# Optimization experiments

Hardware: AMD Instinct MI355X
Metric: run time of the kernel (lower is better)

## Reference

```python
import jax, jax.numpy as jnp
import numpy as np

TEMPERATURE = 0.07
THRESHOLD = 0.7
NUM = 21          # config['data_loader']['args']['class_num']
EPS = 1e-12       # F.normalize eps
NEG_BIG = 1e30


def _nearest_down(x, H, W):
    # torch F.interpolate(mode='nearest'): in_idx = floor(out_idx * in/out)
    Hin, Win = x.shape[-2], x.shape[-1]
    ih = (jnp.arange(H) * Hin) // H
    iw = (jnp.arange(W) * Win) // W
    return x[..., ih[:, None], iw[None, :]]


def _l2n(x):
    return x / jnp.maximum(jnp.linalg.norm(x, axis=1, keepdims=True), EPS)


def setup_inputs() -> dict:
    key = jax.random.key(0)
    ks = jax.random.split(key, 6)
    B, C, H, W = 8, 256, 128, 128
    return {
        "labels": jax.random.randint(ks[0], (B, 512, 512), 0, NUM, dtype=jnp.int64)
        if jax.config.jax_enable_x64 else jax.random.randint(ks[0], (B, 512, 512), 0, NUM, dtype=jnp.int32),
        "features_old": jax.random.normal(ks[1], (B, C, H, W), dtype=jnp.float32),
        "features": jax.random.normal(ks[2], (B, C, H, W), dtype=jnp.float32),
        "outputs_old": jax.random.normal(ks[3], (B, 16, 512, 512), dtype=jnp.float32),
        "outputs": jax.random.normal(ks[4], (B, NUM, 512, 512), dtype=jnp.float32),
        "prototypes": jax.random.normal(ks[5], (NUM, C), dtype=jnp.float32),
        "num_class": 21,
        "num_old_class": 16,
        "num_new_class": 5,
        "epoch": 1,
        "train_step": 1,
        "len_epoch": 100,
    }


def reference(labels, features_old, features, outputs_old, outputs, prototypes,
              num_class, num_old_class, num_new_class, epoch, train_step, len_epoch):
    B, C, H, W = features.shape
    f32 = features.dtype

    # pseudo-label construction
    labels_down = _nearest_down(labels, H, W)                      # [B,H,W] int
    bgr_mask = (labels_down == 0).astype(labels_down.dtype)
    oo = jnp.where(outputs_old < THRESHOLD, 0.0, outputs_old)
    old_pred = jnp.argmax(oo, axis=1)                              # [B,512,512]
    old_down = _nearest_down(old_pred, H, W).astype(labels_down.dtype)
    pseudo = old_down * bgr_mask + labels_down                     # [B,H,W]
    lab = pseudo.reshape(-1)                                       # [N]
    mask = (lab >= 0) & (lab < NUM)

    # [N, C] normalized pixel features
    fa = _l2n(features.transpose(0, 2, 3, 1).reshape(-1, C))
    fo = _l2n(features_old.transpose(0, 2, 3, 1).reshape(-1, C))

    # per-class mean (segment reduce) replacing the python loop over unique labels
    seg = jnp.where(mask, lab, NUM)
    w = mask.astype(f32)
    counts = jax.ops.segment_sum(w, seg, num_segments=NUM + 1)[:NUM]          # [K]
    sum_a = jax.ops.segment_sum(fa * w[:, None], seg, num_segments=NUM + 1)[:NUM]
    sum_o = jax.ops.segment_sum(fo * w[:, None], seg, num_segments=NUM + 1)[:NUM]
    present = counts > 0
    denom = jnp.where(present, counts, 1.0)[:, None]
    anc = jnp.where(present[:, None], sum_a / denom, 0.0)          # [K,C] anchor prototypes
    con_prev = jnp.where(present[:, None], sum_o / denom, 0.0)     # [K,C] old prototypes
    contrast = jax.lax.stop_gradient(jnp.concatenate([anc, con_prev], axis=0))  # [2K,C]

    K = NUM
    eye = jnp.eye(K, dtype=f32)
    rowp = present.astype(f32)                                     # [K]
    colp = jnp.concatenate([rowp, rowp])                           # [2K]
    # labels are unique per row, so R = [I | I]; pos = [0 | I]; neg = 1 - R
    pos_mask = jnp.concatenate([jnp.zeros((K, K), f32), eye], axis=1) * rowp[:, None] * colp[None, :]
    neg_mask = (1.0 - jnp.concatenate([eye, eye], axis=1)) * rowp[:, None] * colp[None, :]

    adc = (anc @ contrast.T) / TEMPERATURE                         # [K,2K]
    # NOTE: faithful to source, negatives use UNshifted logits
    neg = jnp.sum(jnp.exp(adc) * neg_mask, axis=1, keepdims=True)  # [K,1]
    logits_max = jnp.max(jnp.where(colp[None, :] > 0, adc, -NEG_BIG), axis=1, keepdims=True)
    shifted = adc - jax.lax.stop_gradient(logits_max)
    pos_contrast = shifted * pos_mask - jnp.log(jnp.exp(shifted) + neg) * pos_mask

    num = pos_mask.sum(axis=1)
    valid = num > 0
    row_loss = -pos_contrast.sum(axis=1) / jnp.where(valid, num, 1.0)
    loss = jnp.sum(jnp.where(valid, row_loss, 0.0)) / jnp.maximum(jnp.sum(valid.astype(f32)), 1.0)
    return loss
```

## Files before the change

### kernel.cpp

```cpp
#include <hip/hip_runtime.h>
#include <math.h>

#define NPIX   131072
#define CCH    256
#define HW     16384
#define BSTR   4194304
#define NUMC   21
#define KC     5376
#define NREP   16

typedef __attribute__((ext_vector_type(8))) short bf16x8;
typedef __attribute__((ext_vector_type(4))) float f32x4;

static __device__ __forceinline__ uint f2bf(float x) {
    uint u = __builtin_bit_cast(uint, x);
    return (u + 0x7FFFu + ((u >> 16) & 1u)) >> 16;
}
static __device__ __forceinline__ uint oh(int lbl, int cls) {
    return (lbl == cls) ? 0x3F80u : 0u;
}

__global__ __launch_bounds__(256) void k_labels(const int* __restrict__ labels,
                                                const float* __restrict__ outputs_old,
                                                int* __restrict__ lab,
                                                float* __restrict__ gcnt)
{
    __shared__ float cnt[NUMC];
    if (threadIdx.x < NUMC) cnt[threadIdx.x] = 0.f;
    __syncthreads();

    int p = blockIdx.x * 256 + threadIdx.x;
    int b = p >> 14;
    int rem = p & 16383;
    int h = rem >> 7;
    int w = rem & 127;
    int ld = labels[b * 262144 + (h * 4) * 512 + (w * 4)];
    int out = ld;
    if (ld == 0) {
        const float* oo = outputs_old + (size_t)b * BSTR + (size_t)(h * 4) * 512 + (w * 4);
        float v0 = oo[0];
        float best = (v0 < 0.7f) ? 0.0f : v0;
        int bi = 0;
        #pragma unroll
        for (int c = 1; c < 16; ++c) {
            float v = oo[(size_t)c * 262144];
            v = (v < 0.7f) ? 0.0f : v;
            if (v > best) { best = v; bi = c; }
        }
        out = bi;
    }
    lab[p] = out;
    unsafeAtomicAdd(&cnt[out], 1.0f);
    __syncthreads();
    if (threadIdx.x < NUMC) unsafeAtomicAdd(&gcnt[threadIdx.x], cnt[threadIdx.x]);
}

__global__ __launch_bounds__(256, 4) void k_msum(const float* __restrict__ fa,
                                                 const float* __restrict__ fo,
                                                 const int* __restrict__ lab,
                                                 float* __restrict__ partA,
                                                 float* __restrict__ partO)
{
    __shared__ ushort tile[32 * 256];
    __shared__ float4 ssqP4[32];
    __shared__ int    labS[256];

    const int t = threadIdx.x;
    const int w = t >> 6, l = t & 63;
    const int isO = blockIdx.x & 1;
    const float* __restrict__ src = isO ? fo : fa;
    float* part = isO ? partO : partA;

    const int pbase = (blockIdx.x >> 1) * 256;
    const int img   = pbase >> 14;
    const int hw0   = pbase & 16383;
    const float* g  = src + (size_t)img * BSTR + hw0;

    labS[t] = lab[pbase + t];

    const int chb = w * 8 + (l >> 3);
    const int pq  = l & 7;

    f32x4 acc[2][4];
    #pragma unroll
    for (int m = 0; m < 2; ++m)
        #pragma unroll
        for (int n = 0; n < 4; ++n)
            acc[m][n] = (f32x4){0.f, 0.f, 0.f, 0.f};

    float4 v[8];
    #pragma unroll
    for (int i = 0; i < 8; ++i)
        v[i] = *(const float4*)(g + (size_t)(chb + 32 * i) * HW + pq * 4);

    for (int ph = 0; ph < 8; ++ph) {
        float4 s = {0.f, 0.f, 0.f, 0.f};
        #pragma unroll
        for (int i = 0; i < 8; ++i) {
            s.x += v[i].x * v[i].x;  s.y += v[i].y * v[i].y;
            s.z += v[i].z * v[i].z;  s.w += v[i].w * v[i].w;
        }
        #pragma unroll
        for (int off = 8; off < 64; off <<= 1) {
            s.x += __shfl_xor(s.x, off, 64);
            s.y += __shfl_xor(s.y, off, 64);
            s.z += __shfl_xor(s.z, off, 64);
            s.w += __shfl_xor(s.w, off, 64);
        }
        if (l < 8) ssqP4[w * 8 + l] = make_float4(s.x, s.y, s.z, s.w);
        __syncthreads();
        float4 q0 = ssqP4[pq],      q1 = ssqP4[8 + pq];
        float4 q2 = ssqP4[16 + pq], q3 = ssqP4[24 + pq];
        float4 inv;
        inv.x = 1.0f / fmaxf(sqrtf(q0.x + q1.x + q2.x + q3.x), 1e-12f);
        inv.y = 1.0f / fmaxf(sqrtf(q0.y + q1.y + q2.y + q3.y), 1e-12f);
        inv.z = 1.0f / fmaxf(sqrtf(q0.z + q1.z + q2.z + q3.z), 1e-12f);
        inv.w = 1.0f / fmaxf(sqrtf(q0.w + q1.w + q2.w + q3.w), 1e-12f);

        #pragma unroll
        for (int i = 0; i < 8; ++i) {
            uint lo = f2bf(v[i].x * inv.x) | (f2bf(v[i].y * inv.y) << 16);
            uint hi = f2bf(v[i].z * inv.z) | (f2bf(v[i].w * inv.w) << 16);
            int ch = chb + 32 * i;
            *(uint2*)&tile[(((pq >> 1) * 256 + ch) << 3) + ((pq & 1) << 2)] =
                make_uint2(lo, hi);
        }
        if (ph < 7) {
            #pragma unroll
            for (int i = 0; i < 8; ++i)
                v[i] = *(const float4*)(g + (size_t)(chb + 32 * i) * HW + (ph + 1) * 32 + pq * 4);
        }
        __syncthreads();

        const int base = ph * 32 + ((l >> 4) << 3);
        int4 la = *(const int4*)&labS[base];
        int4 lb = *(const int4*)&labS[base + 4];
        const int cls0 = l & 15, cls1 = 16 + (l & 15);
        uint4 u0, u1;
        u0.x = oh(la.x, cls0) | (oh(la.y, cls0) << 16);
        u0.y = oh(la.z, cls0) | (oh(la.w, cls0) << 16);
        u0.z = oh(lb.x, cls0) | (oh(lb.y, cls0) << 16);
        u0.w = oh(lb.z, cls0) | (oh(lb.w, cls0) << 16);
        u1.x = oh(la.x, cls1) | (oh(la.y, cls1) << 16);
        u1.y = oh(la.z, cls1) | (oh(la.w, cls1) << 16);
        u1.z = oh(lb.x, cls1) | (oh(lb.y, cls1) << 16);
        u1.w = oh(lb.z, cls1) | (oh(lb.w, cls1) << 16);
        bf16x8 A0 = __builtin_bit_cast(bf16x8, u0);
        bf16x8 A1 = __builtin_bit_cast(bf16x8, u1);

        #pragma unroll
        for (int n = 0; n < 4; ++n) {
            const int ct = w * 4 + n;
            const bf16x8 B = *(const bf16x8*)&tile[((l >> 4) * 256 + ct * 16 + (l & 15)) << 3];
            acc[0][n] = __builtin_amdgcn_mfma_f32_16x16x32_bf16(A0, B, acc[0][n], 0, 0, 0);
            acc[1][n] = __builtin_amdgcn_mfma_f32_16x16x32_bf16(A1, B, acc[1][n], 0, 0, 0);
        }
    }

    const int rep = (blockIdx.x >> 1) & (NREP - 1);
    #pragma unroll
    for (int m = 0; m < 2; ++m)
        #pragma unroll
        for (int n = 0; n < 4; ++n) {
            const int col = (w * 4 + n) * 16 + (l & 15);
            #pragma unroll
            for (int r = 0; r < 4; ++r) {
                const int row = m * 16 + (l >> 4) * 4 + r;
                if (row < NUMC)
                    unsafeAtomicAdd(&part[rep * KC + row * 256 + col], acc[m][n][r]);
            }
        }
}

__global__ __launch_bounds__(256) void k_final(const float* __restrict__ partA,
                                               const float* __restrict__ partO,
                                               const float* __restrict__ gcnt,
                                               float* __restrict__ out)
{
    __shared__ float anc[NUMC * 260];
    __shared__ float con[NUMC * 260];
    __shared__ float adc[NUMC * 44];
    __shared__ float cntS[NUMC];
    __shared__ float rowloss[NUMC];
    __shared__ float rowvalid[NUMC];

    if (threadIdx.x < NUMC) cntS[threadIdx.x] = gcnt[threadIdx.x];
    __syncthreads();
    for (int i = threadIdx.x; i < KC; i += 256) {
        float sA = 0.f, sO = 0.f;
        #pragma unroll
        for (int r = 0; r < NREP; ++r) { sA += partA[r * KC + i]; sO += partO[r * KC + i]; }
        int k = i >> 8, c = i & 255;
        float cn = cntS[k];
        bool pr = cn > 0.f;
        float d = pr ? cn : 1.f;
        anc[k * 260 + c] = pr ? sA / d : 0.f;
        con[k * 260 + c] = pr ? sO / d : 0.f;
    }
    __syncthreads();
    for (int pair = threadIdx.x; pair < NUMC * 2 * NUMC; pair += 256) {
        int k = pair / (2 * NUMC);
        int j = pair % (2 * NUMC);
        const float* ar = anc + k * 260;
        const float* br = (j < NUMC) ? (anc + j * 260) : (con + (j - NUMC) * 260);
        float s = 0.f;
        for (int c = 0; c < CCH; c += 4) {
            float4 a4 = *(const float4*)(ar + c);
            float4 b4 = *(const float4*)(br + c);
            s += a4.x * b4.x + a4.y * b4.y + a4.z * b4.z + a4.w * b4.w;
        }
        adc[k * 44 + j] = s / 0.07f;
    }
    __syncthreads();
    if (threadIdx.x < NUMC) {
        int k = threadIdx.x;
        bool pr = cntS[k] > 0.f;
        float neg = 0.f;
        float mx = -1e30f;
        for (int j = 0; j < 2 * NUMC; ++j) {
            int cj = (j < NUMC) ? j : (j - NUMC);
            bool cp = cntS[cj] > 0.f;
            float v = adc[k * 44 + j];
            if (cp) {
                if (v > mx) mx = v;
                if (j != k && j != NUMC + k) neg += expf(v);
            }
        }
        float sh = adc[k * 44 + NUMC + k] - mx;
        float rl = -(sh - logf(expf(sh) + neg));
        rowloss[k] = pr ? rl : 0.f;
        rowvalid[k] = pr ? 1.f : 0.f;
    }
    __syncthreads();
    if (threadIdx.x == 0) {
        float s = 0.f, v = 0.f;
        for (int kk = 0; kk < NUMC; ++kk) { s += rowloss[kk]; v += rowvalid[kk]; }
        out[0] = s / fmaxf(v, 1.f);
    }
}

extern "C" void kernel_launch(void* const* d_in, const int* in_sizes, int n_in,
                              void* d_out, int out_size, void* d_ws, size_t ws_size,
                              hipStream_t stream) {
    const int*   labels      = (const int*)  d_in[0];
    const float* feats_old   = (const float*)d_in[1];
    const float* feats       = (const float*)d_in[2];
    const float* outputs_old = (const float*)d_in[3];

    float* ws    = (float*)d_ws;
    int*   lab   = (int*)ws;
    float* partA = ws + 131072;
    float* partO = partA + NREP * KC;
    float* gcnt  = partO + NREP * KC;

    hipMemsetAsync(partA, 0, (size_t)(2 * NREP * KC + NUMC) * sizeof(float), stream);

    k_labels<<<NPIX / 256, 256, 0, stream>>>(labels, outputs_old, lab, gcnt);
    k_msum  <<<1024, 256, 0, stream>>>(feats, feats_old, lab, partA, partO);
    k_final <<<1, 256, 0, stream>>>(partA, partO, gcnt, (float*)d_out);
}
```

Before: 100.5 us.

## Double-buffer feature loads and fold L2 normalization into one-hot MFMA operand

The feature-sum kernel now keeps two register buffers of loads in flight (prefetch distance two) and double-buffers the shared tile and sum-of-squares arrays, which removes one barrier per phase. Features are stored to the tile unnormalized, and the per-pixel inverse norm is placed into the one-hot A operand instead of scaling each value. This aims to hide global load latency and cut per-element multiplies. The costs are higher register pressure (occupancy hint lowered from 4 to 3), doubled shared memory, and a change in bf16 rounding because the inverse norm is itself rounded to bf16.

```diff
diff --git a/kernel.cpp b/kernel.cpp
--- a/kernel.cpp
+++ b/kernel.cpp
@@ -16,8 +16,8 @@
     uint u = __builtin_bit_cast(uint, x);
     return (u + 0x7FFFu + ((u >> 16) & 1u)) >> 16;
 }
-static __device__ __forceinline__ uint oh(int lbl, int cls) {
-    return (lbl == cls) ? 0x3F80u : 0u;
+static __device__ __forceinline__ uint ohv(int lbl, int cls, uint iv) {
+    return (lbl == cls) ? iv : 0u;
 }
 
 __global__ __launch_bounds__(256) void k_labels(const int* __restrict__ labels,
@@ -55,14 +55,14 @@
     if (threadIdx.x < NUMC) unsafeAtomicAdd(&gcnt[threadIdx.x], cnt[threadIdx.x]);
 }
 
-__global__ __launch_bounds__(256, 4) void k_msum(const float* __restrict__ fa,
+__global__ __launch_bounds__(256, 3) void k_msum(const float* __restrict__ fa,
                                                  const float* __restrict__ fo,
                                                  const int* __restrict__ lab,
                                                  float* __restrict__ partA,
                                                  float* __restrict__ partO)
 {
-    __shared__ ushort tile[32 * 256];
-    __shared__ float4 ssqP4[32];
+    __shared__ ushort tile[2][32 * 256];
+    __shared__ float4 ssqP4[2][32];
     __shared__ int    labS[256];
 
     const int t = threadIdx.x;
@@ -88,74 +88,90 @@
         for (int n = 0; n < 4; ++n)
             acc[m][n] = (f32x4){0.f, 0.f, 0.f, 0.f};
 
-    float4 v[8];
-    #pragma unroll
-    for (int i = 0; i < 8; ++i)
-        v[i] = *(const float4*)(g + (size_t)(chb + 32 * i) * HW + pq * 4);
-
-    for (int ph = 0; ph < 8; ++ph) {
-        float4 s = {0.f, 0.f, 0.f, 0.f};
-        #pragma unroll
-        for (int i = 0; i < 8; ++i) {
-            s.x += v[i].x * v[i].x;  s.y += v[i].y * v[i].y;
-            s.z += v[i].z * v[i].z;  s.w += v[i].w * v[i].w;
-        }
-        #pragma unroll
-        for (int off = 8; off < 64; off <<= 1) {
-            s.x += __shfl_xor(s.x, off, 64);
-            s.y += __shfl_xor(s.y, off, 64);
-            s.z += __shfl_xor(s.z, off, 64);
-            s.w += __shfl_xor(s.w, off, 64);
-        }
-        if (l < 8) ssqP4[w * 8 + l] = make_float4(s.x, s.y, s.z, s.w);
-        __syncthreads();
-        float4 q0 = ssqP4[pq],      q1 = ssqP4[8 + pq];
-        float4 q2 = ssqP4[16 + pq], q3 = ssqP4[24 + pq];
-        float4 inv;
-        inv.x = 1.0f / fmaxf(sqrtf(q0.x + q1.x + q2.x + q3.x), 1e-12f);
-        inv.y = 1.0f / fmaxf(sqrtf(q0.y + q1.y + q2.y + q3.y), 1e-12f);
-        inv.z = 1.0f / fmaxf(sqrtf(q0.z + q1.z + q2.z + q3.z), 1e-12f);
-        inv.w = 1.0f / fmaxf(sqrtf(q0.w + q1.w + q2.w + q3.w), 1e-12f);
-
-        #pragma unroll
-        for (int i = 0; i < 8; ++i) {
-            uint lo = f2bf(v[i].x * inv.x) | (f2bf(v[i].y * inv.y) << 16);
-            uint hi = f2bf(v[i].z * inv.z) | (f2bf(v[i].w * inv.w) << 16);
-            int ch = chb + 32 * i;
-            *(uint2*)&tile[(((pq >> 1) * 256 + ch) << 3) + ((pq & 1) << 2)] =
-                make_uint2(lo, hi);
-        }
-        if (ph < 7) {
-            #pragma unroll
-            for (int i = 0; i < 8; ++i)
-                v[i] = *(const float4*)(g + (size_t)(chb + 32 * i) * HW + (ph + 1) * 32 + pq * 4);
-        }
-        __syncthreads();
-
-        const int base = ph * 32 + ((l >> 4) << 3);
-        int4 la = *(const int4*)&labS[base];
-        int4 lb = *(const int4*)&labS[base + 4];
-        const int cls0 = l & 15, cls1 = 16 + (l & 15);
-        uint4 u0, u1;
-        u0.x = oh(la.x, cls0) | (oh(la.y, cls0) << 16);
-        u0.y = oh(la.z, cls0) | (oh(la.w, cls0) << 16);
-        u0.z = oh(lb.x, cls0) | (oh(lb.y, cls0) << 16);
-        u0.w = oh(lb.z, cls0) | (oh(lb.w, cls0) << 16);
-        u1.x = oh(la.x, cls1) | (oh(la.y, cls1) << 16);
-        u1.y = oh(la.z, cls1) | (oh(la.w, cls1) << 16);
-        u1.z = oh(lb.x, cls1) | (oh(lb.y, cls1) << 16);
-        u1.w = oh(lb.z, cls1) | (oh(lb.w, cls1) << 16);
-        bf16x8 A0 = __builtin_bit_cast(bf16x8, u0);
-        bf16x8 A1 = __builtin_bit_cast(bf16x8, u1);
-
-        #pragma unroll
-        for (int n = 0; n < 4; ++n) {
-            const int ct = w * 4 + n;
-            const bf16x8 B = *(const bf16x8*)&tile[((l >> 4) * 256 + ct * 16 + (l & 15)) << 3];
-            acc[0][n] = __builtin_amdgcn_mfma_f32_16x16x32_bf16(A0, B, acc[0][n], 0, 0, 0);
-            acc[1][n] = __builtin_amdgcn_mfma_f32_16x16x32_bf16(A1, B, acc[1][n], 0, 0, 0);
-        }
-    }
+#define ISSUE(buf, ph) do { \
+    _Pragma("unroll") \
+    for (int i_ = 0; i_ < 8; ++i_) \
+        buf[i_] = *(const float4*)(g + (size_t)(chb + 32 * i_) * HW + (ph) * 32 + pq * 4); \
+    } while (0)
+
+#define PHASE(buf, ph, par, pf) do { \
+     \
+    float sx = 0.f, sy = 0.f, sz = 0.f, sw_ = 0.f; \
+    _Pragma("unroll") \
+    for (int i_ = 0; i_ < 8; ++i_) { \
+        sx += buf[i_].x * buf[i_].x;  sy += buf[i_].y * buf[i_].y; \
+        sz += buf[i_].z * buf[i_].z;  sw_ += buf[i_].w * buf[i_].w; \
+    } \
+    _Pragma("unroll") \
+    for (int off_ = 8; off_ < 64; off_ <<= 1) { \
+        sx += __shfl_xor(sx, off_, 64);  sy += __shfl_xor(sy, off_, 64); \
+        sz += __shfl_xor(sz, off_, 64);  sw_ += __shfl_xor(sw_, off_, 64); \
+    } \
+    if (l < 8) ssqP4[par][w * 8 + l] = make_float4(sx, sy, sz, sw_); \
+     \
+    _Pragma("unroll") \
+    for (int i_ = 0; i_ < 8; ++i_) { \
+        uint lo_ = f2bf(buf[i_].x) | (f2bf(buf[i_].y) << 16); \
+        uint hi_ = f2bf(buf[i_].z) | (f2bf(buf[i_].w) << 16); \
+        int ch_ = chb + 32 * i_; \
+        *(uint2*)&tile[par][(((pq >> 1) * 256 + ch_) << 3) + ((pq & 1) << 2)] = \
+            make_uint2(lo_, hi_); \
+    } \
+    if (pf) ISSUE(buf, (ph) + 2); \
+    __syncthreads(); \
+     \
+    const int qd_ = (l >> 4) * 2; \
+    float4 a0_ = ssqP4[par][qd_],      a1_ = ssqP4[par][8 + qd_]; \
+    float4 a2_ = ssqP4[par][16 + qd_], a3_ = ssqP4[par][24 + qd_]; \
+    float4 b0_ = ssqP4[par][qd_ + 1],  b1_ = ssqP4[par][9 + qd_]; \
+    float4 b2_ = ssqP4[par][17 + qd_], b3_ = ssqP4[par][25 + qd_]; \
+    uint iv0 = f2bf(1.f / fmaxf(sqrtf(a0_.x + a1_.x + a2_.x + a3_.x), 1e-12f)); \
+    uint iv1 = f2bf(1.f / fmaxf(sqrtf(a0_.y + a1_.y + a2_.y + a3_.y), 1e-12f)); \
+    uint iv2 = f2bf(1.f / fmaxf(sqrtf(a0_.z + a1_.z + a2_.z + a3_.z), 1e-12f)); \
+    uint iv3 = f2bf(1.f / fmaxf(sqrtf(a0_.w + a1_.w + a2_.w + a3_.w), 1e-12f)); \
+    uint iv4 = f2bf(1.f / fmaxf(sqrtf(b0_.x + b1_.x + b2_.x + b3_.x), 1e-12f)); \
+    uint iv5 = f2bf(1.f / fmaxf(sqrtf(b0_.y + b1_.y + b2_.y + b3_.y), 1e-12f)); \
+    uint iv6 = f2bf(1.f / fmaxf(sqrtf(b0_.z + b1_.z + b2_.z + b3_.z), 1e-12f)); \
+    uint iv7 = f2bf(1.f / fmaxf(sqrtf(b0_.w + b1_.w + b2_.w + b3_.w), 1e-12f)); \
+     \
+    int4 la_ = *(const int4*)&labS[(ph) * 32 + (l >> 4) * 8]; \
+    int4 lb_ = *(const int4*)&labS[(ph) * 32 + (l >> 4) * 8 + 4]; \
+    const int cls0_ = l & 15, cls1_ = 16 + (l & 15); \
+    uint4 u0_, u1_; \
+    u0_.x = ohv(la_.x, cls0_, iv0) | (ohv(la_.y, cls0_, iv1) << 16); \
+    u0_.y = ohv(la_.z, cls0_, iv2) | (ohv(la_.w, cls0_, iv3) << 16); \
+    u0_.z = ohv(lb_.x, cls0_, iv4) | (ohv(lb_.y, cls0_, iv5) << 16); \
+    u0_.w = ohv(lb_.z, cls0_, iv6) | (ohv(lb_.w, cls0_, iv7) << 16); \
+    u1_.x = ohv(la_.x, cls1_, iv0) | (ohv(la_.y, cls1_, iv1) << 16); \
+    u1_.y = ohv(la_.z, cls1_, iv2) | (ohv(la_.w, cls1_, iv3) << 16); \
+    u1_.z = ohv(lb_.x, cls1_, iv4) | (ohv(lb_.y, cls1_, iv5) << 16); \
+    u1_.w = ohv(lb_.z, cls1_, iv6) | (ohv(lb_.w, cls1_, iv7) << 16); \
+    bf16x8 A0_ = __builtin_bit_cast(bf16x8, u0_); \
+    bf16x8 A1_ = __builtin_bit_cast(bf16x8, u1_); \
+    _Pragma("unroll") \
+    for (int n_ = 0; n_ < 4; ++n_) { \
+        const int ct_ = w * 4 + n_; \
+        const bf16x8 B_ = *(const bf16x8*)&tile[par][((l >> 4) * 256 + ct_ * 16 + (l & 15)) << 3]; \
+        acc[0][n_] = __builtin_amdgcn_mfma_f32_16x16x32_bf16(A0_, B_, acc[0][n_], 0, 0, 0); \
+        acc[1][n_] = __builtin_amdgcn_mfma_f32_16x16x32_bf16(A1_, B_, acc[1][n_], 0, 0, 0); \
+    } \
+    } while (0)
+
+    float4 v0[8], v1[8];
+    ISSUE(v0, 0);
+    ISSUE(v1, 1);
+
+    PHASE(v0, 0, 0, 1);
+    PHASE(v1, 1, 1, 1);
+    PHASE(v0, 2, 0, 1);
+    PHASE(v1, 3, 1, 1);
+    PHASE(v0, 4, 0, 1);
+    PHASE(v1, 5, 1, 1);
+    PHASE(v0, 6, 0, 0);
+    PHASE(v1, 7, 1, 0);
+
+#undef ISSUE
+#undef PHASE
 
     const int rep = (blockIdx.x >> 1) & (NREP - 1);
     #pragma unroll
```

New measurement: 100.6 us. About the same (+0.1%).
